# Kernel optimization log

Hardware: AMD Instinct MI355X
Metric: run time of the kernel (lower is better)

## Reference

```python
import math
import jax, jax.numpy as jnp
import numpy as np

EMBED_DIM = 1024
NUM_HEADS = 16
TGT_LEN = 2048
BSZ = 2


def setup_inputs() -> dict:
    key = jax.random.key(0)
    ks = jax.random.split(key, 5)
    E = EMBED_DIM
    # xavier_uniform for in_proj_weight: bound = sqrt(6/(3E+E))
    bw = math.sqrt(6.0 / (3 * E + E))
    in_proj_weight = jax.random.uniform(ks[0], (3 * E, E), jnp.float32, -bw, bw)
    in_proj_bias = jnp.zeros((3 * E,), jnp.float32)
    # out_proj: default Linear init (kaiming-uniform-ish); use uniform(-1/sqrt(E), 1/sqrt(E))
    bo = 1.0 / math.sqrt(E)
    out_w = jax.random.uniform(ks[1], (E, E), jnp.float32, -bo, bo)
    out_b = jnp.zeros((E,), jnp.float32)
    query = jax.random.normal(ks[2], (TGT_LEN, BSZ, E), jnp.float32)
    key_t = jax.random.normal(ks[3], (TGT_LEN, BSZ, E), jnp.float32)
    value = jax.random.normal(ks[4], (TGT_LEN, BSZ, E), jnp.float32)
    return {"query": query, "key": key_t, "value": value,
            "in_proj_weight": in_proj_weight, "in_proj_bias": in_proj_bias,
            "out_w": out_w, "out_b": out_b}


def reference(query, key, value, in_proj_weight, in_proj_bias, out_w, out_b):
    tgt_len, bsz, E = query.shape
    src_len = key.shape[0]
    H = NUM_HEADS
    D = E // H
    # NOTE: original module derives q, k, AND v from `query` (likely a bug kept faithfully)
    qkv = query @ in_proj_weight.T + in_proj_bias  # (T, B, 3E)
    q, k, v = jnp.split(qkv, 3, axis=-1)
    # (len, B*H, D) -> (B*H, len, D)
    q = q.reshape(tgt_len, bsz * H, D).transpose(1, 0, 2)
    k = k.reshape(src_len, bsz * H, D).transpose(1, 0, 2)
    v = v.reshape(src_len, bsz * H, D).transpose(1, 0, 2)
    attn_weights = jnp.einsum('ntd,nsd->nts', q, k) / math.sqrt(D)  # (B*H, T, S)
    attn_weights = jax.nn.softmax(attn_weights, axis=-1)
    attn = jnp.einsum('nts,nsd->ntd', attn_weights, v)  # (B*H, T, D)
    attn = attn.transpose(1, 0, 2).reshape(tgt_len, bsz, E)
    attn = attn @ out_w.T + out_b
    return attn, attn_weights
```

## Files before the change

### kernel.cpp

```cpp
#include <hip/hip_runtime.h>

typedef unsigned short ushortT;
typedef unsigned int uintT;
typedef __attribute__((ext_vector_type(8))) short bf16x8;
typedef __attribute__((ext_vector_type(16))) float f32x16;
typedef __attribute__((ext_vector_type(4))) unsigned short ushort4v;
typedef __attribute__((ext_vector_type(2))) unsigned short ushort2v;

constexpr int T_LEN = 2048;
constexpr int BSZ_C = 2;
constexpr int E_C   = 1024;
constexpr int H_C   = 16;
constexpr int NH    = 32;
constexpr int E3    = 3072;
constexpr int M_C   = T_LEN * BSZ_C;

static __device__ inline ushortT f2bf(float f) {
    union { float f; uintT u; } v; v.f = f;
    uintT u = v.u;
    return (ushortT)((u + 0x7fffu + ((u >> 16) & 1u)) >> 16);
}
static __device__ inline f32x16 mfma_bf16(bf16x8 a, bf16x8 b, f32x16 c) {
    return __builtin_amdgcn_mfma_f32_32x32x16_bf16(a, b, c, 0, 0, 0);
}
static __device__ inline void gload_lds16(const ushortT* g, ushortT* l) {
    __builtin_amdgcn_global_load_lds(
        (const __attribute__((address_space(1))) void*)g,
        (__attribute__((address_space(3))) void*)l, 16, 0, 0);
}

constexpr int Q4C  = M_C * E_C / 4;
constexpr int WI4C = E3 * E_C / 4;
constexpr int WO4C = E_C * E_C / 4;

__global__ __launch_bounds__(256) void pack3(const float* __restrict__ query,
                                             const float* __restrict__ W_in,
                                             const float* __restrict__ W_out,
                                             ushortT* __restrict__ qh,
                                             ushortT* __restrict__ Wih,
                                             ushortT* __restrict__ Woh)
{
    const int total = Q4C + WI4C + WO4C;
    const int stride = gridDim.x * 256;
    for (int i = blockIdx.x * 256 + threadIdx.x; i < total; i += stride) {
        const float4* src;
        ushortT* dst;
        int j;
        if (i < Q4C)              { src = (const float4*)query; dst = qh;  j = i; }
        else if (i < Q4C + WI4C)  { src = (const float4*)W_in;  dst = Wih; j = i - Q4C; }
        else                      { src = (const float4*)W_out; dst = Woh; j = i - Q4C - WI4C; }
        float4 v = src[j];
        ushort4v h;
        h.x = f2bf(v.x); h.y = f2bf(v.y); h.z = f2bf(v.z); h.w = f2bf(v.w);
        *(ushort4v*)(dst + (size_t)j * 4) = h;
    }
}

__global__ __launch_bounds__(256) void gemm_bf16_qkv(const ushortT* __restrict__ Ah,
                                                     const ushortT* __restrict__ Bh,
                                                     const float* __restrict__ bias,
                                                     ushortT* __restrict__ qh_o,
                                                     ushortT* __restrict__ kh_o,
                                                     ushortT* __restrict__ vt_o)
{
    const int K = E_C;
    __shared__ ushortT As[128][64];
    __shared__ ushortT Bs[128][64];

    const int tid = threadIdx.x;
    const int bm = blockIdx.y * 128, bn = blockIdx.x * 128;
    const int w  = tid >> 6;
    const int wm = w >> 1, wn = w & 1;
    const int l  = tid & 63;
    const int lc = l & 31, hi = l >> 5;

    f32x16 acc[2][2];
    #pragma unroll
    for (int a = 0; a < 2; a++)
        #pragma unroll
        for (int b = 0; b < 2; b++)
            #pragma unroll
            for (int r = 0; r < 16; r++) acc[a][b][r] = 0.f;

    for (int k0 = 0; k0 < K; k0 += 64) {
        #pragma unroll
        for (int it = 0; it < 4; it++) {
            int idx = it * 256 + (w << 6) + l;
            int row = idx >> 3;
            int cs  = (idx & 7) ^ (row & 7);
            size_t goff = (size_t)row * K + k0 + cs * 8;
            int lbase = (it * 256 + (w << 6)) * 8;
            gload_lds16(Ah + (size_t)bm * K + goff, &As[0][0] + lbase);
            gload_lds16(Bh + (size_t)bn * K + goff, &Bs[0][0] + lbase);
        }
        __syncthreads();

        #pragma unroll
        for (int ks = 0; ks < 4; ks++) {
            bf16x8 af[2], bfr[2];
            #pragma unroll
            for (int ms = 0; ms < 2; ms++) {
                int r = wm * 64 + ms * 32 + lc;
                af[ms] = *(const bf16x8*)(&As[r][(((ks << 1) + hi) ^ (r & 7)) << 3]);
            }
            #pragma unroll
            for (int ns = 0; ns < 2; ns++) {
                int r = wn * 64 + ns * 32 + lc;
                bfr[ns] = *(const bf16x8*)(&Bs[r][(((ks << 1) + hi) ^ (r & 7)) << 3]);
            }
            #pragma unroll
            for (int ms = 0; ms < 2; ms++)
                #pragma unroll
                for (int ns = 0; ns < 2; ns++)
                    acc[ms][ns] = mfma_bf16(af[ms], bfr[ns], acc[ms][ns]);
        }
        __syncthreads();
    }

    const bool is_v = (bn >= 2048);
    #pragma unroll
    for (int ms = 0; ms < 2; ms++)
        #pragma unroll
        for (int ns = 0; ns < 2; ns++) {
            int col = bn + wn * 64 + ns * 32 + lc;
            float bcol = bias[col];
            if (is_v) {
                int cc = col & 1023, hh = cc >> 6, dd = cc & 63;
                #pragma unroll
                for (int rq = 0; rq < 8; rq++) {
                    int r = (rq & 1) + 4 * (rq >> 1);
                    int rowb = bm + wm * 64 + ms * 32 + 8 * (r >> 2) + 4 * hi;
                    int bb = r & 1;
                    int t = rowb >> 1;
                    int nhead = bb * H_C + hh;
                    ushort2v p;
                    p.x = f2bf(acc[ms][ns][r] + bcol);
                    p.y = f2bf(acc[ms][ns][r + 2] + bcol);
                    *(ushort2v*)(vt_o + ((size_t)nhead * 64 + dd) * T_LEN + t) = p;
                }
            } else {
                ushortT* dst = (col < 1024) ? qh_o : kh_o;
                int cc = col & 1023, hh = cc >> 6, dd = cc & 63;
                #pragma unroll
                for (int r = 0; r < 16; r++) {
                    int row = bm + wm * 64 + ms * 32 + (r & 3) + 8 * (r >> 2) + 4 * hi;
                    int t = row >> 1, bb = row & 1;
                    int nhead = bb * H_C + hh;
                    dst[((size_t)nhead * T_LEN + t) * 64 + dd] = f2bf(acc[ms][ns][r] + bcol);
                }
            }
        }
}

__global__ __launch_bounds__(256) void gemm_bf16_out(const ushortT* __restrict__ Ah,
                                                     const ushortT* __restrict__ Bh,
                                                     const float* __restrict__ bias,
                                                     float* __restrict__ Cf)
{
    const int K = E_C, N = E_C;
    __shared__ ushortT As[128][64];
    __shared__ ushortT Bs[128][64];

    const int tid = threadIdx.x;
    const int bm = blockIdx.y * 128, bn = blockIdx.x * 128;
    const int w  = tid >> 6;
    const int wm = w >> 1, wn = w & 1;
    const int l  = tid & 63;
    const int lc = l & 31, hi = l >> 5;

    f32x16 acc[2][2];
    #pragma unroll
    for (int a = 0; a < 2; a++)
        #pragma unroll
        for (int b = 0; b < 2; b++)
            #pragma unroll
            for (int r = 0; r < 16; r++) acc[a][b][r] = 0.f;

    for (int k0 = 0; k0 < K; k0 += 64) {
        #pragma unroll
        for (int it = 0; it < 4; it++) {
            int idx = it * 256 + (w << 6) + l;
            int row = idx >> 3;
            int cs  = (idx & 7) ^ (row & 7);
            size_t goff = (size_t)row * K + k0 + cs * 8;
            int lbase = (it * 256 + (w << 6)) * 8;
            gload_lds16(Ah + (size_t)bm * K + goff, &As[0][0] + lbase);
            gload_lds16(Bh + (size_t)bn * K + goff, &Bs[0][0] + lbase);
        }
        __syncthreads();

        #pragma unroll
        for (int ks = 0; ks < 4; ks++) {
            bf16x8 af[2], bfr[2];
            #pragma unroll
            for (int ms = 0; ms < 2; ms++) {
                int r = wm * 64 + ms * 32 + lc;
                af[ms] = *(const bf16x8*)(&As[r][(((ks << 1) + hi) ^ (r & 7)) << 3]);
            }
            #pragma unroll
            for (int ns = 0; ns < 2; ns++) {
                int r = wn * 64 + ns * 32 + lc;
                bfr[ns] = *(const bf16x8*)(&Bs[r][(((ks << 1) + hi) ^ (r & 7)) << 3]);
            }
            #pragma unroll
            for (int ms = 0; ms < 2; ms++)
                #pragma unroll
                for (int ns = 0; ns < 2; ns++)
                    acc[ms][ns] = mfma_bf16(af[ms], bfr[ns], acc[ms][ns]);
        }
        __syncthreads();
    }

    #pragma unroll
    for (int ms = 0; ms < 2; ms++)
        #pragma unroll
        for (int ns = 0; ns < 2; ns++)
            #pragma unroll
            for (int r = 0; r < 16; r++) {
                int row = bm + wm * 64 + ms * 32 + (r & 3) + 8 * (r >> 2) + 4 * hi;
                int col = bn + wn * 64 + ns * 32 + lc;
                __builtin_nontemporal_store(acc[ms][ns][r] + bias[col],
                                            &Cf[(size_t)row * N + col]);
            }
}

__global__ __launch_bounds__(256) void attn_mfma(const ushortT* __restrict__ q_h,
                                                 const ushortT* __restrict__ k_h,
                                                 const ushortT* __restrict__ v_t,
                                                 float* __restrict__ p_out,
                                                 ushortT* __restrict__ a_hi)
{
    __shared__ ushortT plds[4][32][64];

    const int n = blockIdx.x;
    const int b = n >> 4, h = n & 15;
    const int t0 = blockIdx.y * 128;
    const int tid = threadIdx.x;
    const int w = tid >> 6, l = tid & 63;
    const int lc = l & 31, hi = l >> 5;
    const int trow_base = t0 + w * 32;

    const ushortT* qb = q_h + ((size_t)n * T_LEN + trow_base) * 64;
    const ushortT* kb = k_h + (size_t)n * T_LEN * 64;
    const ushortT* vb = v_t + (size_t)n * 64 * T_LEN;

    bf16x8 qf[4];
    #pragma unroll
    for (int ks = 0; ks < 4; ks++)
        qf[ks] = *(const bf16x8*)(qb + (size_t)lc * 64 + ks * 16 + hi * 8);

    const float scale = 0.125f;

    float sum[16];
    #pragma unroll
    for (int r = 0; r < 16; r++) sum[r] = 0.f;

    for (int s0 = 0; s0 < T_LEN; s0 += 32) {
        const ushortT* kr = kb + (size_t)(s0 + lc) * 64 + hi * 8;
        f32x16 c;
        #pragma unroll
        for (int r = 0; r < 16; r++) c[r] = 0.f;
        #pragma unroll
        for (int ks = 0; ks < 4; ks++)
            c = mfma_bf16(qf[ks], *(const bf16x8*)(kr + ks * 16), c);
        #pragma unroll
        for (int r = 0; r < 16; r++) sum[r] += __expf(c[r] * scale);
    }
    #pragma unroll
    for (int r = 0; r < 16; r++) {
        float s = sum[r];
        s += __shfl_xor(s, 1, 64);
        s += __shfl_xor(s, 2, 64);
        s += __shfl_xor(s, 4, 64);
        s += __shfl_xor(s, 8, 64);
        s += __shfl_xor(s, 16, 64);
        sum[r] = 1.0f / s;
    }

    f32x16 o0, o1;
    #pragma unroll
    for (int r = 0; r < 16; r++) { o0[r] = 0.f; o1[r] = 0.f; }
    char* plbase = (char*)&plds[w][0][0];

    for (int s0 = 0; s0 < T_LEN; s0 += 32) {
        const ushortT* kr = kb + (size_t)(s0 + lc) * 64 + hi * 8;
        f32x16 c;
        #pragma unroll
        for (int r = 0; r < 16; r++) c[r] = 0.f;
        #pragma unroll
        for (int ks = 0; ks < 4; ks++)
            c = mfma_bf16(qf[ks], *(const bf16x8*)(kr + ks * 16), c);

        float pv[16];
        #pragma unroll
        for (int r = 0; r < 16; r++) pv[r] = __expf(c[r] * scale) * sum[r];

        size_t pbase = ((size_t)n * T_LEN) * T_LEN + s0 + lc;
        #pragma unroll
        for (int r = 0; r < 16; r++) {
            int t = trow_base + (r & 3) + 8 * (r >> 2) + 4 * hi;
            __builtin_nontemporal_store(pv[r], &p_out[pbase + (size_t)t * T_LEN]);
        }
        #pragma unroll
        for (int r = 0; r < 16; r++) {
            int row = (r & 3) + 8 * (r >> 2) + 4 * hi;
            int byte = row * 128 + ((lc * 2) ^ ((row & 7) << 4));
            *(ushortT*)(plbase + byte) = f2bf(pv[r]);
        }
        bf16x8 pa[2];
        #pragma unroll
        for (int sh = 0; sh < 2; sh++) {
            int S = (hi * 8 + sh * 16) * 2;
            int byte = lc * 128 + (S ^ ((lc & 7) << 4));
            pa[sh] = *(const bf16x8*)(plbase + byte);
        }
        #pragma unroll
        for (int sh = 0; sh < 2; sh++) {
            bf16x8 v0 = *(const bf16x8*)(vb + (size_t)(lc) * T_LEN + s0 + sh * 16 + hi * 8);
            bf16x8 v1 = *(const bf16x8*)(vb + (size_t)(32 + lc) * T_LEN + s0 + sh * 16 + hi * 8);
            o0 = mfma_bf16(pa[sh], v0, o0);
            o1 = mfma_bf16(pa[sh], v1, o1);
        }
    }

    #pragma unroll
    for (int r = 0; r < 16; r++) {
        int t = trow_base + (r & 3) + 8 * (r >> 2) + 4 * hi;
        size_t m = (size_t)t * BSZ_C + b;
        size_t base = m * 1024 + h * 64;
        a_hi[base + lc]      = f2bf(o0[r]);
        a_hi[base + 32 + lc] = f2bf(o1[r]);
    }
}

extern "C" void kernel_launch(void* const* d_in, const int* in_sizes, int n_in,
                              void* d_out, int out_size, void* d_ws, size_t ws_size,
                              hipStream_t stream) {
    const float* query = (const float*)d_in[0];
    const float* W_in  = (const float*)d_in[3];
    const float* b_in  = (const float*)d_in[4];
    const float* W_out = (const float*)d_in[5];
    const float* b_out = (const float*)d_in[6];

    float* out   = (float*)d_out;
    float* p_out = out + (size_t)T_LEN * BSZ_C * E_C;

    char* ws = (char*)d_ws;
    ushortT* qh   = (ushortT*)(ws + 0);
    ushortT* Wih  = (ushortT*)(ws + 8388608);
    ushortT* Woh  = (ushortT*)(ws + 14680064);
    ushortT* q_h  = (ushortT*)(ws + 16777216);
    ushortT* k_h  = (ushortT*)(ws + 25165824);
    ushortT* v_t  = (ushortT*)(ws + 33554432);
    ushortT* a_hi = (ushortT*)(ws + 41943040);

    dim3 blk(256);

    pack3<<<dim3(2048), blk, 0, stream>>>(query, W_in, W_out, qh, Wih, Woh);

    gemm_bf16_qkv<<<dim3(E3 / 128, M_C / 128), blk, 0, stream>>>(
        qh, Wih, b_in, q_h, k_h, v_t);

    attn_mfma<<<dim3(NH, T_LEN / 128), blk, 0, stream>>>(q_h, k_h, v_t, p_out, a_hi);

    gemm_bf16_out<<<dim3(E_C / 128, M_C / 128), blk, 0, stream>>>(
        a_hi, Woh, b_out, out);
}
```

Baseline: 293.9 us.

## Split attention key range across two wave groups and vectorize probability stores

The attention kernel now runs 512 threads per block, and two groups of four waves each take half of the source sequence. Softmax denominators and output partials are combined through LDS with block barriers. The attention-probability output is read back from the bf16 LDS tile and written as coalesced float4 nontemporal stores, replacing the scattered scalar stores. This also means stored probabilities are bf16-rounded. exp is computed as exp2f with a prescaled constant. The changes aim to raise parallelism and store efficiency at the cost of extra LDS (obuf 32KB) and syncs.

```diff
diff --git a/kernel.cpp b/kernel.cpp
--- a/kernel.cpp
+++ b/kernel.cpp
@@ -4,6 +4,7 @@
 typedef unsigned int uintT;
 typedef __attribute__((ext_vector_type(8))) short bf16x8;
 typedef __attribute__((ext_vector_type(16))) float f32x16;
+typedef __attribute__((ext_vector_type(4))) float f32x4;
 typedef __attribute__((ext_vector_type(4))) unsigned short ushort4v;
 typedef __attribute__((ext_vector_type(2))) unsigned short ushort2v;
 
@@ -224,21 +225,25 @@
             }
 }
 
-__global__ __launch_bounds__(256) void attn_mfma(const ushortT* __restrict__ q_h,
-                                                 const ushortT* __restrict__ k_h,
-                                                 const ushortT* __restrict__ v_t,
-                                                 float* __restrict__ p_out,
-                                                 ushortT* __restrict__ a_hi)
+__global__ __launch_bounds__(512, 4) void attn_mfma(const ushortT* __restrict__ q_h,
+                                                    const ushortT* __restrict__ k_h,
+                                                    const ushortT* __restrict__ v_t,
+                                                    float* __restrict__ p_out,
+                                                    ushortT* __restrict__ a_hi)
 {
-    __shared__ ushortT plds[4][32][64];
+    __shared__ ushortT plds[8][32][64];
+    __shared__ float sums_lds[2][4][32];
+    __shared__ float obuf[4][32][64];
 
     const int n = blockIdx.x;
     const int b = n >> 4, h = n & 15;
     const int t0 = blockIdx.y * 128;
     const int tid = threadIdx.x;
     const int w = tid >> 6, l = tid & 63;
+    const int rg = w & 3, s2 = w >> 2;
     const int lc = l & 31, hi = l >> 5;
-    const int trow_base = t0 + w * 32;
+    const int trow_base = t0 + rg * 32;
+    const int sbase = s2 * 1024;
 
     const ushortT* qb = q_h + ((size_t)n * T_LEN + trow_base) * 64;
     const ushortT* kb = k_h + (size_t)n * T_LEN * 64;
@@ -249,13 +254,14 @@
     for (int ks = 0; ks < 4; ks++)
         qf[ks] = *(const bf16x8*)(qb + (size_t)lc * 64 + ks * 16 + hi * 8);
 
-    const float scale = 0.125f;
+    const float K2 = 0.18033688011112042f;
 
     float sum[16];
     #pragma unroll
     for (int r = 0; r < 16; r++) sum[r] = 0.f;
 
-    for (int s0 = 0; s0 < T_LEN; s0 += 32) {
+    #pragma unroll 2
+    for (int s0 = sbase; s0 < sbase + 1024; s0 += 32) {
         const ushortT* kr = kb + (size_t)(s0 + lc) * 64 + hi * 8;
         f32x16 c;
         #pragma unroll
@@ -264,7 +270,7 @@
         for (int ks = 0; ks < 4; ks++)
             c = mfma_bf16(qf[ks], *(const bf16x8*)(kr + ks * 16), c);
         #pragma unroll
-        for (int r = 0; r < 16; r++) sum[r] += __expf(c[r] * scale);
+        for (int r = 0; r < 16; r++) sum[r] += exp2f(c[r] * K2);
     }
     #pragma unroll
     for (int r = 0; r < 16; r++) {
@@ -274,7 +280,21 @@
         s += __shfl_xor(s, 4, 64);
         s += __shfl_xor(s, 8, 64);
         s += __shfl_xor(s, 16, 64);
-        sum[r] = 1.0f / s;
+        sum[r] = s;
+    }
+    if (lc == 0) {
+        #pragma unroll
+        for (int r = 0; r < 16; r++) {
+            int row32 = (r & 3) + 8 * (r >> 2) + 4 * hi;
+            sums_lds[s2][rg][row32] = sum[r];
+        }
+    }
+    __syncthreads();
+    float inv[16];
+    #pragma unroll
+    for (int r = 0; r < 16; r++) {
+        int row32 = (r & 3) + 8 * (r >> 2) + 4 * hi;
+        inv[r] = 1.0f / (sums_lds[0][rg][row32] + sums_lds[1][rg][row32]);
     }
 
     f32x16 o0, o1;
@@ -282,7 +302,7 @@
     for (int r = 0; r < 16; r++) { o0[r] = 0.f; o1[r] = 0.f; }
     char* plbase = (char*)&plds[w][0][0];
 
-    for (int s0 = 0; s0 < T_LEN; s0 += 32) {
+    for (int s0 = sbase; s0 < sbase + 1024; s0 += 32) {
         const ushortT* kr = kb + (size_t)(s0 + lc) * 64 + hi * 8;
         f32x16 c;
         #pragma unroll
@@ -291,22 +311,30 @@
         for (int ks = 0; ks < 4; ks++)
             c = mfma_bf16(qf[ks], *(const bf16x8*)(kr + ks * 16), c);
 
-        float pv[16];
-        #pragma unroll
-        for (int r = 0; r < 16; r++) pv[r] = __expf(c[r] * scale) * sum[r];
-
-        size_t pbase = ((size_t)n * T_LEN) * T_LEN + s0 + lc;
         #pragma unroll
         for (int r = 0; r < 16; r++) {
-            int t = trow_base + (r & 3) + 8 * (r >> 2) + 4 * hi;
-            __builtin_nontemporal_store(pv[r], &p_out[pbase + (size_t)t * T_LEN]);
-        }
-        #pragma unroll
-        for (int r = 0; r < 16; r++) {
+            float pv = exp2f(c[r] * K2) * inv[r];
             int row = (r & 3) + 8 * (r >> 2) + 4 * hi;
             int byte = row * 128 + ((lc * 2) ^ ((row & 7) << 4));
-            *(ushortT*)(plbase + byte) = f2bf(pv[r]);
-        }
+            *(ushortT*)(plbase + byte) = f2bf(pv);
+        }
+
+        #pragma unroll
+        for (int j = 0; j < 4; j++) {
+            int row = (l >> 3) + 8 * j;
+            int c4  = l & 7;
+            int byte = row * 128 + ((c4 * 8) ^ ((row & 7) << 4));
+            uint2 d = *(const uint2*)(plbase + byte);
+            f32x4 f;
+            union { uintT u; float f; } cv;
+            cv.u = d.x << 16;         f.x = cv.f;
+            cv.u = d.x & 0xffff0000u; f.y = cv.f;
+            cv.u = d.y << 16;         f.z = cv.f;
+            cv.u = d.y & 0xffff0000u; f.w = cv.f;
+            float* dst = p_out + ((size_t)n * T_LEN + trow_base + row) * T_LEN + s0 + c4 * 4;
+            __builtin_nontemporal_store(f, (f32x4*)dst);
+        }
+
         bf16x8 pa[2];
         #pragma unroll
         for (int sh = 0; sh < 2; sh++) {
@@ -323,13 +351,23 @@
         }
     }
 
-    #pragma unroll
-    for (int r = 0; r < 16; r++) {
-        int t = trow_base + (r & 3) + 8 * (r >> 2) + 4 * hi;
-        size_t m = (size_t)t * BSZ_C + b;
-        size_t base = m * 1024 + h * 64;
-        a_hi[base + lc]      = f2bf(o0[r]);
-        a_hi[base + 32 + lc] = f2bf(o1[r]);
+    if (s2 == 1) {
+        #pragma unroll
+        for (int j = 0; j < 16; j++) obuf[rg][j][l] = o0[j];
+        #pragma unroll
+        for (int j = 0; j < 16; j++) obuf[rg][16 + j][l] = o1[j];
+    }
+    __syncthreads();
+    if (s2 == 0) {
+        #pragma unroll
+        for (int r = 0; r < 16; r++) {
+            float x0 = o0[r] + obuf[rg][r][l];
+            float x1 = o1[r] + obuf[rg][16 + r][l];
+            int t = trow_base + (r & 3) + 8 * (r >> 2) + 4 * hi;
+            size_t base = ((size_t)t * BSZ_C + b) * 1024 + h * 64;
+            a_hi[base + lc]      = f2bf(x0);
+            a_hi[base + 32 + lc] = f2bf(x1);
+        }
     }
 }
 
@@ -354,15 +392,14 @@
     ushortT* v_t  = (ushortT*)(ws + 33554432);
     ushortT* a_hi = (ushortT*)(ws + 41943040);
 
-    dim3 blk(256);
-
-    pack3<<<dim3(2048), blk, 0, stream>>>(query, W_in, W_out, qh, Wih, Woh);
-
-    gemm_bf16_qkv<<<dim3(E3 / 128, M_C / 128), blk, 0, stream>>>(
+    pack3<<<dim3(2048), dim3(256), 0, stream>>>(query, W_in, W_out, qh, Wih, Woh);
+
+    gemm_bf16_qkv<<<dim3(E3 / 128, M_C / 128), dim3(256), 0, stream>>>(
         qh, Wih, b_in, q_h, k_h, v_t);
 
-    attn_mfma<<<dim3(NH, T_LEN / 128), blk, 0, stream>>>(q_h, k_h, v_t, p_out, a_hi);
-
-    gemm_bf16_out<<<dim3(E_C / 128, M_C / 128), blk, 0, stream>>>(
+    attn_mfma<<<dim3(NH, T_LEN / 128), dim3(512), 0, stream>>>(
+        q_h, k_h, v_t, p_out, a_hi);
+
+    gemm_bf16_out<<<dim3(E_C / 128, M_C / 128), dim3(256), 0, stream>>>(
         a_hi, Woh, b_out, out);
 }
```

Result: slower. 307.3 us (+4.6%).
